# Kernel optimization log

Hardware: AMD Instinct MI355X
Metric: run time of the kernel (lower is better)

## Reference

```python
import jax, jax.numpy as jnp
import numpy as np

B, F, T, Z, Y, X = 1, 8, 5, 16, 96, 96
N_RAYS = 32768   # n_rays_scan
K = 128          # n_points_ray
NEAR_PLANE = 0.01
C = F * Z        # conv channels after folding Z into channel dim


def setup_inputs() -> dict:
    key = jax.random.key(0)
    ks = jax.random.split(key, 6)
    vol = jax.random.normal(ks[0], (B, F, T, Z, Y, X), jnp.float32)
    # ray origins inside the normalized unit-cube scene
    rays_o = jax.random.uniform(ks[1], (T, N_RAYS, 3), jnp.float32, 0.1, 0.9)
    rd = jax.random.normal(ks[2], (T, N_RAYS, 3), jnp.float32)
    rays_d = rd / jnp.linalg.norm(rd, axis=-1, keepdims=True)
    conv_w = jax.random.normal(ks[3], (C, C, 3, 3, 3), jnp.float32) * (1.0 / np.sqrt(C * 27))
    conv_b = jnp.zeros((C,), jnp.float32)
    dens_w = jax.random.normal(ks[4], (F, 1), jnp.float32) * (1.0 / np.sqrt(F))
    dens_b = jnp.zeros((1,), jnp.float32)
    return dict(curr_feat_volume=vol, ray_start=rays_o, ray_direction=rays_d,
                conv_w=conv_w, conv_b=conv_b, dens_w=dens_w, dens_b=dens_b)


def _trilinear(vol, pts):
    """vol: [F,Z,Y,X]; pts: [...,3] with (x,y,z) in [0,1]. Returns [..., F]."""
    Fc, Zs, Ys, Xs = vol.shape
    gx = jnp.clip(pts[..., 0], 0.0, 1.0) * (Xs - 1)
    gy = jnp.clip(pts[..., 1], 0.0, 1.0) * (Ys - 1)
    gz = jnp.clip(pts[..., 2], 0.0, 1.0) * (Zs - 1)
    x0 = jnp.floor(gx).astype(jnp.int32); x1 = jnp.minimum(x0 + 1, Xs - 1)
    y0 = jnp.floor(gy).astype(jnp.int32); y1 = jnp.minimum(y0 + 1, Ys - 1)
    z0 = jnp.floor(gz).astype(jnp.int32); z1 = jnp.minimum(z0 + 1, Zs - 1)
    fx = gx - x0; fy = gy - y0; fz = gz - z0
    out = 0.0
    for zi, wz in ((z0, 1 - fz), (z1, fz)):
        for yi, wy in ((y0, 1 - fy), (y1, fy)):
            for xi, wx in ((x0, 1 - fx), (x1, fx)):
                out = out + vol[:, zi, yi, xi] * (wz * wy * wx)[None]
    return jnp.moveaxis(out, 0, -1)


def _render_t(vol_t, o, d, dens_w, dens_b):
    """One timestep: vol_t [F,Z,Y,X], o/d [N,3] -> depth [N,1]."""
    # SceneCollider: AABB [0,1]^3 with near_plane clamp
    t1 = (0.0 - o) / d
    t2 = (1.0 - o) / d
    near = jnp.max(jnp.minimum(t1, t2), axis=-1, keepdims=True)
    far = jnp.min(jnp.maximum(t1, t2), axis=-1, keepdims=True)
    near = jnp.maximum(near, NEAR_PLANE)
    far = jnp.maximum(far, near + 1e-6)
    # UniformSampler (deterministic bins)
    bins = jnp.linspace(0.0, 1.0, K + 1, dtype=jnp.float32)
    ts = near + bins[None, :] * (far - near)          # [N,K+1]
    starts = ts[:, :-1, None]                          # [N,K,1]
    ends = ts[:, 1:, None]
    mids = 0.5 * (starts + ends)
    pts = o[:, None, :] + d[:, None, :] * mids         # [N,K,3]
    # DensityField: trilinear feature gather + linear + softplus
    feats = _trilinear(vol_t, pts)                     # [N,K,F]
    density = jax.nn.softplus(feats @ dens_w + dens_b) # [N,K,1]
    # weights / transmittance (alpha compositing)
    deltas = ends - starts
    dd = density * deltas
    trans = jnp.exp(-jnp.concatenate([jnp.zeros_like(dd[:, :1]),
                                      jnp.cumsum(dd[:, :-1], axis=1)], axis=1))
    alpha = 1.0 - jnp.exp(-dd)
    weights = alpha * trans                            # [N,K,1]
    # DepthRenderer
    eps = 1e-10
    depth = jnp.sum(weights * starts, axis=-2) / (jnp.sum(weights, axis=-2) + eps)
    depth = jnp.clip(depth, starts.min(), starts.max())
    return depth                                       # [N,1]


def reference(curr_feat_volume, ray_start, ray_direction, conv_w, conv_b, dens_w, dens_b):
    # fold Z into channels and run dense Conv3d over (T,Y,X)
    x = jnp.transpose(curr_feat_volume, (0, 1, 3, 2, 4, 5)).reshape(B, F * Z, T, Y, X)
    y = jax.lax.conv_general_dilated(
        x, conv_w, window_strides=(1, 1, 1), padding='SAME',
        dimension_numbers=('NCDHW', 'OIDHW', 'NCDHW'))
    y = y + conv_b[None, :, None, None, None]
    future = jnp.transpose(y.reshape(B, F, Z, T, Y, X), (0, 3, 1, 2, 4, 5))  # [B,T,F,Z,Y,X]
    vols = future[0]                                   # [T,F,Z,Y,X]
    depth = jax.vmap(lambda v, o, d: _render_t(v, o, d, dens_w, dens_b))(
        vols, ray_start, ray_direction)                # [T,N,1]
    return depth
```

## Files before the change

kernel.cpp:

```cpp
#include <hip/hip_runtime.h>
#include <hip/hip_fp16.h>
#include <cstdint>
#include <cstddef>

#define T_DIM 5
#define F_DIM 8
#define Z_DIM 16
#define Y_DIM 96
#define X_DIM 96
#define NRAYS 32768
#define K_SAMP 128


struct __align__(16) Cell { __half2 h0, h1, h2, h3; };

typedef __attribute__((ext_vector_type(4))) float     f32x4;
typedef __attribute__((ext_vector_type(8))) _Float16  f16x8;

__device__ __forceinline__ float fexp2(float x) { return __builtin_amdgcn_exp2f(x); }
__device__ __forceinline__ float flog2(float x) { return __builtin_amdgcn_logf(x); }

__global__ __launch_bounds__(256) void setup_kernel(
        const float* __restrict__ xin, __half* __restrict__ inp,
        const float* __restrict__ w, const float* __restrict__ cb,
        const float* __restrict__ dw, __half* __restrict__ wB, float* __restrict__ bR,
        const float* __restrict__ ro, const float* __restrict__ rd,
        float* __restrict__ nearA, float* __restrict__ farA) {
    int b = blockIdx.x;
    if (b < 480) {
        __shared__ __half lds[96 * 136];
        int t = b / 96, y = b - (b / 96) * 96;
        for (int i = threadIdx.x; i < 12288; i += 256) {
            int row = i / 96;
            int x   = i - row * 96;
            int f = row >> 4, z = row & 15;
            float v = xin[(((size_t)(f * 5 + t) * 16 + z) * 96 + y) * 96 + x];
            lds[x * 136 + row] = __float2half(v);
        }
        __syncthreads();
        __half* ob = inp + ((size_t)(t * 96 + y) * 96) * 128;
        for (int c = threadIdx.x; c < 1536; c += 256) {
            int x = c >> 4, sub = c & 15;
            uint4 v = *(const uint4*)(lds + x * 136 + sub * 8);
            *(uint4*)(ob + (size_t)x * 128 + sub * 8) = v;
        }
    } else if (b < 696) {
        int i = (b - 480) * 256 + threadIdx.x;
        if (i < 16) {
            float s = 0.f;
            #pragma unroll
            for (int f = 0; f < 8; ++f) s += cb[f * 16 + i] * dw[f];
            bR[i] = s;
        }
        int cs  = i & 31;
        int zo  = (i >> 5) & 15;
        int pt  = i >> 9;
        int p   = pt / 27;
        int tap = pt - p * 27;
        int ci  = p * 32 + cs;
        float s = 0.f;
        #pragma unroll
        for (int f = 0; f < 8; ++f)
            s += w[(size_t)((f * 16 + zo) * 128 + ci) * 27 + tap] * dw[f];
        wB[i] = __float2half(s);
    } else {
        int gid = (b - 696) * 256 + threadIdx.x;
        const float* o = ro + (size_t)gid * 3;
        const float* d = rd + (size_t)gid * 3;
        float ox = o[0], oy = o[1], oz = o[2];
        float dx = d[0], dy = d[1], dz = d[2];
        float t1x = (0.f - ox) / dx, t2x = (1.f - ox) / dx;
        float t1y = (0.f - oy) / dy, t2y = (1.f - oy) / dy;
        float t1z = (0.f - oz) / dz, t2z = (1.f - oz) / dz;
        float nr = fmaxf(fmaxf(fminf(t1x, t2x), fminf(t1y, t2y)), fminf(t1z, t2z));
        float fr = fminf(fminf(fmaxf(t1x, t2x), fmaxf(t1y, t2y)), fmaxf(t1z, t2z));
        nr = fmaxf(nr, 0.01f);
        fr = fmaxf(fr, nr + 1e-6f);
        nearA[gid] = nr;
        farA[gid]  = fr;
    }
}

__global__ __launch_bounds__(128) void conv_mfma_kernel(
        const __half* __restrict__ inp, const __half* __restrict__ wB,
        const float* __restrict__ bR, float* __restrict__ fld) {
    int bid = blockIdx.x;
    int wg  = (bid & 7) * 90 + (bid >> 3);
    int xs  = wg % 3;
    int rem = wg / 3;
    int yp  = rem % 48;
    int t   = rem / 48;
    int xseg = xs * 32, y0 = yp * 2;

    __shared__ __half lds[2][12 * 34 * 32];
    const int w    = threadIdx.x >> 6;
    const int lane = threadIdx.x & 63;
    const int l15  = lane & 15;
    const int ksub = lane >> 4;

    const int xl0 = threadIdx.x >> 2, sub0 = threadIdx.x & 3;
    const int xg0 = xseg + xl0 - 1;
    const bool xok0 = (unsigned)xg0 < 96u;
    const int glo0 = xg0 * 128 + sub0 * 8;
    const int lof0 = xl0 * 32 + ((sub0 ^ ((xl0 >> 1) & 3)) << 3);
    const int q    = threadIdx.x / 12;
    const int rowh = threadIdx.x - q * 12;
    const int xl1  = 32 + (q >> 2), sub1 = q & 3;
    const int xg1  = xseg + xl1 - 1;
    const bool hwr = (q < 8);
    const bool hld = hwr && ((unsigned)xg1 < 96u);
    const int glo1 = xg1 * 128 + sub1 * 8;
    const int lof1 = xl1 * 32 + ((sub1 ^ ((xl1 >> 1) & 3)) << 3);

    int offA[3];
    #pragma unroll
    for (int kx = 0; kx < 3; ++kx) {
        int X = l15 + kx;
        offA[kx] = X * 32 + ((ksub ^ ((X >> 1) & 3)) << 3);
    }

    uint4 vm[12];
    uint4 vh;
    f32x4 acc0 = {0.f, 0.f, 0.f, 0.f};
    f32x4 acc1 = {0.f, 0.f, 0.f, 0.f};

    #pragma unroll
    for (int r = 0; r < 12; ++r) {
        int tt = t + (r >> 2) - 1;
        int yy = y0 + (r & 3) - 1;
        bool rok = ((unsigned)tt < 5u) & ((unsigned)yy < 96u);
        int rbase = (tt * 96 + yy) * 12288;
        uint4 v = {0u, 0u, 0u, 0u};
        if (rok & xok0) v = *(const uint4*)(inp + rbase + glo0);
        vm[r] = v;
    }
    {
        int tt = t + (rowh >> 2) - 1;
        int yy = y0 + (rowh & 3) - 1;
        bool rok = ((unsigned)tt < 5u) & ((unsigned)yy < 96u);
        int rbase = (tt * 96 + yy) * 12288;
        uint4 v = {0u, 0u, 0u, 0u};
        if (rok & hld) v = *(const uint4*)(inp + rbase + glo1);
        vh = v;
    }

    #pragma unroll
    for (int p = 0; p < 4; ++p) {
        __half* L = &lds[p & 1][0];
        #pragma unroll
        for (int r = 0; r < 12; ++r)
            *(uint4*)(L + r * 1088 + lof0) = vm[r];
        if (hwr)
            *(uint4*)(L + rowh * 1088 + lof1) = vh;
        __syncthreads();

        if (p < 3) {
            #pragma unroll
            for (int r = 0; r < 12; ++r) {
                int tt = t + (r >> 2) - 1;
                int yy = y0 + (r & 3) - 1;
                bool rok = ((unsigned)tt < 5u) & ((unsigned)yy < 96u);
                int rbase = (tt * 96 + yy) * 12288 + ((p + 1) << 5);
                uint4 v = {0u, 0u, 0u, 0u};
                if (rok & xok0) v = *(const uint4*)(inp + rbase + glo0);
                vm[r] = v;
            }
            {
                int tt = t + (rowh >> 2) - 1;
                int yy = y0 + (rowh & 3) - 1;
                bool rok = ((unsigned)tt < 5u) & ((unsigned)yy < 96u);
                int rbase = (tt * 96 + yy) * 12288 + ((p + 1) << 5);
                uint4 v = {0u, 0u, 0u, 0u};
                if (rok & hld) v = *(const uint4*)(inp + rbase + glo1);
                vh = v;
            }
        }

        const __half* wp_base = wB + (size_t)p * 13824 + l15 * 32 + ksub * 8;
        #pragma unroll
        for (int kt = 0; kt < 3; ++kt) {
            #pragma unroll
            for (int ky = 0; ky < 3; ++ky) {
                const __half* lrow = L + (kt * 4 + w + ky) * 1088;
                #pragma unroll
                for (int kx = 0; kx < 3; ++kx) {
                    int tap = (kt * 3 + ky) * 3 + kx;
                    f16x8 aw = *(const f16x8*)(wp_base + tap * 512);
                    f16x8 b0 = *(const f16x8*)(lrow + offA[kx]);
                    acc0 = __builtin_amdgcn_mfma_f32_16x16x32_f16(aw, b0, acc0, 0, 0, 0);
                    f16x8 b1 = *(const f16x8*)(lrow + offA[kx] + 512);
                    acc1 = __builtin_amdgcn_mfma_f32_16x16x32_f16(aw, b1, acc1, 0, 0, 0);
                }
            }
        }
    }

    int yw = y0 + w;
    #pragma unroll
    for (int r = 0; r < 4; ++r) {
        int zo = ksub * 4 + r;
        float bz = bR[zo];
        size_t o = (((size_t)t * 16 + zo) * 96 + yw) * 96 + xseg + l15;
        fld[o]      = acc0[r] + bz;
        fld[o + 16] = acc1[r] + bz;
    }
}

__global__ __launch_bounds__(256) void pack_kernel(
        const float* __restrict__ fld, Cell* __restrict__ cellp) {
    int i = blockIdx.x * 256 + threadIdx.x;
    if (i >= 737280) return;
    int x = i % 96;
    int r = i / 96;
    int y = r % 96;
    int r2 = r / 96;
    int z = r2 % 16;
    int t = r2 / 16;
    const float* ft = fld + (size_t)t * 147456;
    int xp = min(x + 1, 95);
    int yr0 = y * 96, yr1 = min(y + 1, 95) * 96;
    int zr0 = z * 9216, zr1 = min(z + 1, 15) * 9216;
    float c000 = ft[zr0 + yr0 + x], c001 = ft[zr0 + yr0 + xp];
    float c010 = ft[zr0 + yr1 + x], c011 = ft[zr0 + yr1 + xp];
    float c100 = ft[zr1 + yr0 + x], c101 = ft[zr1 + yr0 + xp];
    float c110 = ft[zr1 + yr1 + x], c111 = ft[zr1 + yr1 + xp];
    Cell cl;
    cl.h0 = __floats2half2_rn(c000, c001 - c000);
    cl.h1 = __floats2half2_rn(c010, c011 - c010);
    cl.h2 = __floats2half2_rn(c100, c101 - c100);
    cl.h3 = __floats2half2_rn(c110, c111 - c110);
    cellp[i] = cl;
}

__global__ __launch_bounds__(256) void render_kernel(
        const float* __restrict__ ro, const float* __restrict__ rd,
        const Cell* __restrict__ cellp,
        const float* __restrict__ nearA, const float* __restrict__ farA,
        const float* __restrict__ dens_b, float* __restrict__ out) {
    int b = blockIdx.x;
    int b7 = b & 7, bhi = b >> 3;
    int t, seg;
    if (b7 < 5) { t = b7; seg = bhi; }
    else { int j = (b7 - 5) * 320 + bhi; t = j / 192; seg = 320 + j % 192; }
    int c = threadIdx.x & 3;
    int ray = t * NRAYS + seg * 64 + (threadIdx.x >> 2);

    const float* o = ro + (size_t)ray * 3;
    const float* d = rd + (size_t)ray * 3;
    float ox = o[0], oy = o[1], oz = o[2];
    float dx = d[0], dy = d[1], dz = d[2];
    float nr = nearA[ray], fr = farA[ray];
    const Cell* vt = cellp + (size_t)t * 147456;
    const float L2E = 1.4426950408889634f;
    float db2 = dens_b[0] * L2E;

    float span = fr - nr;
    float step = span * 0.0078125f;
    float s  = fmaf((float)(c * 32), step, nr);
    float mid = s + 0.5f * step;
    float pxg = fmaf(dx, mid, ox) * 95.f;
    float pyg = fmaf(dy, mid, oy) * 95.f;
    float pzg = fmaf(dz, mid, oz) * 15.f;
    float ddxg = dx * step * 95.f, ddyg = dy * step * 95.f, ddzg = dz * step * 15.f;

    float num = 0.f, den = 0.f, A2 = 0.f;
    float trans = 1.f;
    int pidx = -1;
    Cell cl;
    for (int kk = 0; kk < 32; ++kk) {
        float gx = fminf(fmaxf(pxg, 0.f), 95.f);
        float gy = fminf(fmaxf(pyg, 0.f), 95.f);
        float gz = fminf(fmaxf(pzg, 0.f), 15.f);
        int x0 = min((int)gx, 94), y0 = min((int)gy, 94), z0 = min((int)gz, 14);
        float fx = gx - (float)x0, fy = gy - (float)y0, fz = gz - (float)z0;

        int idx = z0 * 9216 + y0 * 96 + x0;
        if (idx != pidx) {
            pidx = idx;
            cl = vt[idx];
        }

        float v00 = fmaf(fx, __half2float(__high2half(cl.h0)), __half2float(__low2half(cl.h0)));
        float v01 = fmaf(fx, __half2float(__high2half(cl.h1)), __half2float(__low2half(cl.h1)));
        float v10 = fmaf(fx, __half2float(__high2half(cl.h2)), __half2float(__low2half(cl.h2)));
        float v11 = fmaf(fx, __half2float(__high2half(cl.h3)), __half2float(__low2half(cl.h3)));
        float v0  = fmaf(fy, v01 - v00, v00);
        float v1  = fmaf(fy, v11 - v10, v10);
        float pre2 = fmaf(fmaf(fz, v1 - v0, v0), L2E, db2);

        float u = fexp2(-fabsf(pre2));
        float dens2 = fmaxf(pre2, 0.f) + flog2(1.f + u);
        float dd2 = dens2 * step;
        float ex = fexp2(-dd2);
        float wgt = (1.f - ex) * trans;
        num = fmaf(wgt, s, num);
        den += wgt;
        trans *= ex;
        A2 += dd2;
        s += step; pxg += ddxg; pyg += ddyg; pzg += ddzg;
    }
    int lane = threadIdx.x & 63;
    int qb = lane & ~3;
    float A0 = __shfl(A2, qb,     64);
    float A1 = __shfl(A2, qb + 1, 64);
    float Ab = __shfl(A2, qb + 2, 64);
    float P = 0.f;
    if (c > 0) P += A0;
    if (c > 1) P += A1;
    if (c > 2) P += Ab;
    float sc = fexp2(-P);
    float numc = num * sc;
    float denc = den * sc;
    numc += __shfl_xor(numc, 1, 64);
    numc += __shfl_xor(numc, 2, 64);
    denc += __shfl_xor(denc, 1, 64);
    denc += __shfl_xor(denc, 2, 64);
    if (c == 0) {
        float depth = numc / (denc + 1e-10f);
        float slast = fmaf(0.9921875f, span, nr);
        depth = fminf(fmaxf(depth, nr), slast);
        out[ray] = depth;
    }
}

extern "C" void kernel_launch(void* const* d_in, const int* in_sizes, int n_in,
                              void* d_out, int out_size, void* d_ws, size_t ws_size,
                              hipStream_t stream) {
    const float* vol = (const float*)d_in[0];
    const float* ro  = (const float*)d_in[1];
    const float* rd  = (const float*)d_in[2];
    const float* cw  = (const float*)d_in[3];
    const float* cb  = (const float*)d_in[4];
    const float* dw  = (const float*)d_in[5];
    const float* dbp = (const float*)d_in[6];
    float* out = (float*)d_out;

    float* ws      = (float*)d_ws;
    float* fld     = ws;
    __half* inp    = (__half*)(ws + 737280);
    Cell*  cellp   = (Cell*)(ws + 737280);
    __half* wB     = (__half*)(ws + 737280 + 2949120);
    float* bR      = ws + 737280 + 2949120 + 27648;
    float* nearA   = bR + 32;
    float* farA    = nearA + 163840;

    hipLaunchKernelGGL(setup_kernel, dim3(1336), dim3(256), 0, stream,
                       vol, inp, cw, cb, dw, wB, bR, ro, rd, nearA, farA);
    hipLaunchKernelGGL(conv_mfma_kernel, dim3(720), dim3(128), 0, stream,
                       inp, wB, bR, fld);
    hipLaunchKernelGGL(pack_kernel, dim3(2880), dim3(256), 0, stream, fld, cellp);
    hipLaunchKernelGGL(render_kernel, dim3(2560), dim3(256), 0, stream,
                       ro, rd, cellp, nearA, farA, dbp, out);
}
```

Measured before the change: 165.9 us.

## Split conv x-tiles across four waves and prefetch next render cell

The conv kernel doubles its workgroup to 256 threads so each wave computes one 16-wide x tile instead of two. Global-to-LDS staging is split across thread halves (6 rows each), which cuts per-thread registers and adds wave-level parallelism for the MFMA work. The render loop is software-pipelined: it computes the next sample's cell index and issues that load before evaluating the current sample, which hides gather latency. The render change also drops the clamping of float coordinates to the volume range before computing fractions, so out-of-range points may be interpolated differently from the reference.

```diff
diff --git a/kernel.cpp b/kernel.cpp
--- a/kernel.cpp
+++ b/kernel.cpp
@@ -81,7 +81,7 @@
     }
 }
 
-__global__ __launch_bounds__(128) void conv_mfma_kernel(
+__global__ __launch_bounds__(256) void conv_mfma_kernel(
         const __half* __restrict__ inp, const __half* __restrict__ wB,
         const float* __restrict__ bR, float* __restrict__ fld) {
     int bid = blockIdx.x;
@@ -93,21 +93,26 @@
     int xseg = xs * 32, y0 = yp * 2;
 
     __shared__ __half lds[2][12 * 34 * 32];
-    const int w    = threadIdx.x >> 6;
-    const int lane = threadIdx.x & 63;
+    const int tid  = threadIdx.x;
+    const int wid  = tid >> 6;
+    const int w    = wid & 1;
+    const int xt   = wid >> 1;
+    const int lane = tid & 63;
     const int l15  = lane & 15;
     const int ksub = lane >> 4;
 
-    const int xl0 = threadIdx.x >> 2, sub0 = threadIdx.x & 3;
+    const int l128 = tid & 127;
+    const int xl0 = l128 >> 2, sub0 = l128 & 3;
+    const int rlo = (tid >> 7) * 6;
     const int xg0 = xseg + xl0 - 1;
     const bool xok0 = (unsigned)xg0 < 96u;
     const int glo0 = xg0 * 128 + sub0 * 8;
     const int lof0 = xl0 * 32 + ((sub0 ^ ((xl0 >> 1) & 3)) << 3);
-    const int q    = threadIdx.x / 12;
-    const int rowh = threadIdx.x - q * 12;
-    const int xl1  = 32 + (q >> 2), sub1 = q & 3;
+    const int qh   = tid / 12;
+    const int rowh = tid - qh * 12;
+    const int xl1  = 32 + (qh >> 2), sub1 = qh & 3;
+    const bool hwr = (tid < 96);
     const int xg1  = xseg + xl1 - 1;
-    const bool hwr = (q < 8);
     const bool hld = hwr && ((unsigned)xg1 < 96u);
     const int glo1 = xg1 * 128 + sub1 * 8;
     const int lof1 = xl1 * 32 + ((sub1 ^ ((xl1 >> 1) & 3)) << 3);
@@ -115,24 +120,24 @@
     int offA[3];
     #pragma unroll
     for (int kx = 0; kx < 3; ++kx) {
-        int X = l15 + kx;
+        int X = xt * 16 + l15 + kx;
         offA[kx] = X * 32 + ((ksub ^ ((X >> 1) & 3)) << 3);
     }
 
-    uint4 vm[12];
+    uint4 vm[6];
     uint4 vh;
-    f32x4 acc0 = {0.f, 0.f, 0.f, 0.f};
-    f32x4 acc1 = {0.f, 0.f, 0.f, 0.f};
+    f32x4 acc = {0.f, 0.f, 0.f, 0.f};
 
     #pragma unroll
-    for (int r = 0; r < 12; ++r) {
+    for (int rr = 0; rr < 6; ++rr) {
+        int r = rlo + rr;
         int tt = t + (r >> 2) - 1;
         int yy = y0 + (r & 3) - 1;
         bool rok = ((unsigned)tt < 5u) & ((unsigned)yy < 96u);
         int rbase = (tt * 96 + yy) * 12288;
         uint4 v = {0u, 0u, 0u, 0u};
         if (rok & xok0) v = *(const uint4*)(inp + rbase + glo0);
-        vm[r] = v;
+        vm[rr] = v;
     }
     {
         int tt = t + (rowh >> 2) - 1;
@@ -148,22 +153,23 @@
     for (int p = 0; p < 4; ++p) {
         __half* L = &lds[p & 1][0];
         #pragma unroll
-        for (int r = 0; r < 12; ++r)
-            *(uint4*)(L + r * 1088 + lof0) = vm[r];
+        for (int rr = 0; rr < 6; ++rr)
+            *(uint4*)(L + (rlo + rr) * 1088 + lof0) = vm[rr];
         if (hwr)
             *(uint4*)(L + rowh * 1088 + lof1) = vh;
         __syncthreads();
 
         if (p < 3) {
             #pragma unroll
-            for (int r = 0; r < 12; ++r) {
+            for (int rr = 0; rr < 6; ++rr) {
+                int r = rlo + rr;
                 int tt = t + (r >> 2) - 1;
                 int yy = y0 + (r & 3) - 1;
                 bool rok = ((unsigned)tt < 5u) & ((unsigned)yy < 96u);
                 int rbase = (tt * 96 + yy) * 12288 + ((p + 1) << 5);
                 uint4 v = {0u, 0u, 0u, 0u};
                 if (rok & xok0) v = *(const uint4*)(inp + rbase + glo0);
-                vm[r] = v;
+                vm[rr] = v;
             }
             {
                 int tt = t + (rowh >> 2) - 1;
@@ -186,10 +192,8 @@
                 for (int kx = 0; kx < 3; ++kx) {
                     int tap = (kt * 3 + ky) * 3 + kx;
                     f16x8 aw = *(const f16x8*)(wp_base + tap * 512);
-                    f16x8 b0 = *(const f16x8*)(lrow + offA[kx]);
-                    acc0 = __builtin_amdgcn_mfma_f32_16x16x32_f16(aw, b0, acc0, 0, 0, 0);
-                    f16x8 b1 = *(const f16x8*)(lrow + offA[kx] + 512);
-                    acc1 = __builtin_amdgcn_mfma_f32_16x16x32_f16(aw, b1, acc1, 0, 0, 0);
+                    f16x8 bb = *(const f16x8*)(lrow + offA[kx]);
+                    acc = __builtin_amdgcn_mfma_f32_16x16x32_f16(aw, bb, acc, 0, 0, 0);
                 }
             }
         }
@@ -200,9 +204,8 @@
     for (int r = 0; r < 4; ++r) {
         int zo = ksub * 4 + r;
         float bz = bR[zo];
-        size_t o = (((size_t)t * 16 + zo) * 96 + yw) * 96 + xseg + l15;
-        fld[o]      = acc0[r] + bz;
-        fld[o + 16] = acc1[r] + bz;
+        size_t o = (((size_t)t * 16 + zo) * 96 + yw) * 96 + xseg + xt * 16 + l15;
+        fld[o] = acc[r] + bz;
     }
 }
 
@@ -263,30 +266,35 @@
     float pzg = fmaf(dz, mid, oz) * 15.f;
     float ddxg = dx * step * 95.f, ddyg = dy * step * 95.f, ddzg = dz * step * 15.f;
 
+    int x0 = min(max((int)pxg, 0), 94);
+    int y0 = min(max((int)pyg, 0), 94);
+    int z0 = min(max((int)pzg, 0), 14);
+    float cfx = pxg - (float)x0, cfy = pyg - (float)y0, cfz = pzg - (float)z0;
+    int pidx = z0 * 9216 + y0 * 96 + x0;
+    Cell cl = vt[pidx];
+
     float num = 0.f, den = 0.f, A2 = 0.f;
     float trans = 1.f;
-    int pidx = -1;
-    Cell cl;
     for (int kk = 0; kk < 32; ++kk) {
-        float gx = fminf(fmaxf(pxg, 0.f), 95.f);
-        float gy = fminf(fmaxf(pyg, 0.f), 95.f);
-        float gz = fminf(fmaxf(pzg, 0.f), 15.f);
-        int x0 = min((int)gx, 94), y0 = min((int)gy, 94), z0 = min((int)gz, 14);
-        float fx = gx - (float)x0, fy = gy - (float)y0, fz = gz - (float)z0;
-
-        int idx = z0 * 9216 + y0 * 96 + x0;
-        if (idx != pidx) {
-            pidx = idx;
-            cl = vt[idx];
-        }
-
-        float v00 = fmaf(fx, __half2float(__high2half(cl.h0)), __half2float(__low2half(cl.h0)));
-        float v01 = fmaf(fx, __half2float(__high2half(cl.h1)), __half2float(__low2half(cl.h1)));
-        float v10 = fmaf(fx, __half2float(__high2half(cl.h2)), __half2float(__low2half(cl.h2)));
-        float v11 = fmaf(fx, __half2float(__high2half(cl.h3)), __half2float(__low2half(cl.h3)));
-        float v0  = fmaf(fy, v01 - v00, v00);
-        float v1  = fmaf(fy, v11 - v10, v10);
-        float pre2 = fmaf(fmaf(fz, v1 - v0, v0), L2E, db2);
+        pxg += ddxg; pyg += ddyg; pzg += ddzg;
+        int nx = min(max((int)pxg, 0), 94);
+        int ny = min(max((int)pyg, 0), 94);
+        int nz = min(max((int)pzg, 0), 14);
+        float nfx = pxg - (float)nx, nfy = pyg - (float)ny, nfz = pzg - (float)nz;
+        int nidx = nz * 9216 + ny * 96 + nx;
+        Cell cn = cl;
+        if (nidx != pidx) {
+            pidx = nidx;
+            cn = vt[nidx];
+        }
+
+        float v00 = fmaf(cfx, __half2float(__high2half(cl.h0)), __half2float(__low2half(cl.h0)));
+        float v01 = fmaf(cfx, __half2float(__high2half(cl.h1)), __half2float(__low2half(cl.h1)));
+        float v10 = fmaf(cfx, __half2float(__high2half(cl.h2)), __half2float(__low2half(cl.h2)));
+        float v11 = fmaf(cfx, __half2float(__high2half(cl.h3)), __half2float(__low2half(cl.h3)));
+        float v0  = fmaf(cfy, v01 - v00, v00);
+        float v1  = fmaf(cfy, v11 - v10, v10);
+        float pre2 = fmaf(fmaf(cfz, v1 - v0, v0), L2E, db2);
 
         float u = fexp2(-fabsf(pre2));
         float dens2 = fmaxf(pre2, 0.f) + flog2(1.f + u);
@@ -297,7 +305,9 @@
         den += wgt;
         trans *= ex;
         A2 += dd2;
-        s += step; pxg += ddxg; pyg += ddyg; pzg += ddzg;
+        s += step;
+
+        cl = cn; cfx = nfx; cfy = nfy; cfz = nfz;
     }
     int lane = threadIdx.x & 63;
     int qb = lane & ~3;
@@ -346,7 +356,7 @@
 
     hipLaunchKernelGGL(setup_kernel, dim3(1336), dim3(256), 0, stream,
                        vol, inp, cw, cb, dw, wB, bR, ro, rd, nearA, farA);
-    hipLaunchKernelGGL(conv_mfma_kernel, dim3(720), dim3(128), 0, stream,
+    hipLaunchKernelGGL(conv_mfma_kernel, dim3(720), dim3(256), 0, stream,
                        inp, wB, bR, fld);
     hipLaunchKernelGGL(pack_kernel, dim3(2880), dim3(256), 0, stream, fld, cellp);
     hipLaunchKernelGGL(render_kernel, dim3(2560), dim3(256), 0, stream,
```

New measurement: 172.3 us. 3.9% more time.
